# Performance work log

Hardware: AMD Instinct MI355X
Metric: run time of the kernel (lower is better)

The kernel has to match this reference:

```python
import jax, jax.numpy as jnp
import numpy as np

B, S, D, MAX_LEN = 4, 2048, 512, 2048
V = 2 * MAX_LEN + 1  # embedding table size
POS_MAX = 3000


def setup_inputs() -> dict:
    key = jax.random.key(0)
    k1, k2, k3 = jax.random.split(key, 3)
    x = jax.random.normal(k1, (B, S, D), dtype=jnp.float32)
    emb_table = jax.random.normal(k2, (V, D), dtype=jnp.float32) * 0.02
    positions = jnp.sort(jax.random.randint(k3, (B, S), 0, POS_MAX), axis=-1)
    return {"x": x, "emb_table": emb_table, "positions": positions}


def reference(x, emb_table, positions):
    # x: [B,S,D], emb_table: [2M+1, D], positions: [B,S] int
    Bc, Sc, _ = x.shape
    Vc = emb_table.shape[0]
    M = (Vc - 1) // 2
    # rel[b,i,j] = clamp(pos_i - pos_j, -M, M) + M   -> index into table
    rel = jnp.clip(positions[:, :, None] - positions[:, None, :], -M, M) + M  # [B,S,S]
    # mean_j emb[rel[b,i,j]] == (occurrence counts over V) @ table / S
    # counts[b,i,v] = #{j : rel[b,i,j] == v}; identical math, no [B,S,S,D] tensor.
    b_idx = jnp.arange(Bc)[:, None, None]
    i_idx = jnp.arange(Sc)[None, :, None]
    counts = jnp.zeros((Bc, Sc, Vc), dtype=x.dtype).at[b_idx, i_idx, rel].add(1.0)
    mean_emb = jnp.einsum('bsv,vd->bsd', counts, emb_table) / Sc  # [B,S,D]
    return x + mean_emb
```

## Files before the change

kernel.cpp:

```cpp
#include <hip/hip_runtime.h>
#include <hip/hip_bf16.h>
#include <cstdint>

#define NB 4
#define NS 2048
#define ND 512
#define NM 2048
#define NV 4097
#define NP 3000
#define RSW 3080
#define EBI_KB 129
#define HTI_BATCH_BYTES (2 * 256 * 1024)

typedef __bf16 bf16x8 __attribute__((ext_vector_type(8)));
typedef float f32x4 __attribute__((ext_vector_type(4)));

__device__ __forceinline__ unsigned short f2bf(float f) {
  union { __bf16 b; unsigned short u; } cv;
  cv.b = (__bf16)f;
  return cv.u;
}

__device__ __forceinline__ int lbound_dev(const int* a, int n, int key) {
  int lo = 0, hi = n;
  while (lo < hi) { int mid = (lo + hi) >> 1; if (a[mid] < key) lo = mid + 1; else hi = mid; }
  return lo;
}

__global__ void k_prep(const int* __restrict__ pos, const float* __restrict__ emb,
                       unsigned short* __restrict__ HTI, unsigned short* __restrict__ EBI,
                       int* __restrict__ rs) {
  __shared__ float tile[64][65];
  __shared__ unsigned int h[NP];
  int blk = blockIdx.x, tid = threadIdx.x;
  if (blk < 52) {
    int b = blk & 3, chunk = blk >> 2;
    int t = chunk * 256 + tid;
    if (t <= 3072) rs[b * RSW + t] = lbound_dev(pos + b * NS, NS, t);
    return;
  }
  if (blk < 564) {
    int idx = (blk - 52) * 256 + tid;
    int bb = idx >> 15;
    for (int i = tid; i < NP; i += 256) h[i] = 0u;
    __syncthreads();
    const int* pb = pos + bb * NS;
    for (int i = tid; i < NS; i += 256) atomicAdd(&h[pb[i]], 1u);
    __syncthreads();
    int l = idx & 63;
    int tb = (idx >> 6) & 255;
    int p = (idx >> 14) & 1;
    int base = 5104 + (l & 15) - tb * 32 - p * 16 - ((l >> 4) * 8);
    union { unsigned short us[8]; uint4 v4; } pk;
#pragma unroll
    for (int e = 0; e < 8; ++e) {
      int ii = base - e;
      float f = (ii >= 0 && ii < NP) ? (float)h[ii] : 0.0f;
      pk.us[e] = f2bf(f);
    }
    *(uint4*)(HTI + ((size_t)(bb * 2 + p) * 256 + tb) * 512 + l * 8) = pk.v4;
    return;
  }
  {
    int blk2 = blk - 564;
    int v0 = (blk2 % 65) * 64, d0 = (blk2 / 65) * 64;
    int c = tid & 63, r0 = tid >> 6;
#pragma unroll
    for (int k = 0; k < 16; ++k) {
      int r = k * 4 + r0;
      int v = v0 + r;
      float val = 0.f;
      if (v < NV && v != 0 && v != (NV - 1)) val = emb[(size_t)v * ND + d0 + c];
      tile[r][c] = val;
    }
    __syncthreads();
#pragma unroll
    for (int rep = 0; rep < 2; ++rep) {
      int tile_id = rep * 4 + (tid >> 6);
      int l = tid & 63;
      int kb_loc = tile_id >> 2, dt_loc = tile_id & 3;
      int kb = (v0 >> 5) + kb_loc, dt = (d0 >> 4) + dt_loc;
      if (kb < EBI_KB) {
        union { unsigned short us[8]; uint4 v4; } pk;
#pragma unroll
        for (int e = 0; e < 8; ++e)
          pk.us[e] = f2bf(tile[kb_loc * 32 + ((l >> 4) * 8) + e][dt_loc * 16 + (l & 15)]);
        *(uint4*)(EBI + ((size_t)dt * EBI_KB + kb) * 512 + l * 8) = pk.v4;
      }
    }
  }
}

#define LOADSET(sa0, sa1, sb0, sb1, sb2, sb3, tt)                                   \
  if ((tt) < nt) {                                                                  \
    int tof = (tt) * 1024 + vo;                                                     \
    sa0 = *(const bf16x8*)(hb + (size_t)(cA0 + tof));                               \
    sa1 = *(const bf16x8*)(hb + (size_t)(cA1 + tof));                               \
    sb0 = *(const bf16x8*)(eb + (size_t)(cB0 + tof));                               \
    sb1 = *(const bf16x8*)(eb + (size_t)(cB1 + tof));                               \
    sb2 = *(const bf16x8*)(eb + (size_t)(cB2 + tof));                               \
    sb3 = *(const bf16x8*)(eb + (size_t)(cB3 + tof));                               \
  }

#define MMSET(sa0, sa1, sb0, sb1, sb2, sb3)                                         \
  acc[0][0] = __builtin_amdgcn_mfma_f32_16x16x32_bf16(sa0, sb0, acc[0][0], 0, 0, 0);\
  acc[0][1] = __builtin_amdgcn_mfma_f32_16x16x32_bf16(sa0, sb1, acc[0][1], 0, 0, 0);\
  acc[0][2] = __builtin_amdgcn_mfma_f32_16x16x32_bf16(sa0, sb2, acc[0][2], 0, 0, 0);\
  acc[0][3] = __builtin_amdgcn_mfma_f32_16x16x32_bf16(sa0, sb3, acc[0][3], 0, 0, 0);\
  acc[1][0] = __builtin_amdgcn_mfma_f32_16x16x32_bf16(sa1, sb0, acc[1][0], 0, 0, 0);\
  acc[1][1] = __builtin_amdgcn_mfma_f32_16x16x32_bf16(sa1, sb1, acc[1][1], 0, 0, 0);\
  acc[1][2] = __builtin_amdgcn_mfma_f32_16x16x32_bf16(sa1, sb2, acc[1][2], 0, 0, 0);\
  acc[1][3] = __builtin_amdgcn_mfma_f32_16x16x32_bf16(sa1, sb3, acc[1][3], 0, 0, 0);

__global__ __launch_bounds__(256)
void k4_gemm(const unsigned short* __restrict__ HTI, const unsigned short* __restrict__ EBI,
             const int* __restrict__ rs, const float* __restrict__ x,
             const float* __restrict__ emb, float* __restrict__ out) {
  int tid = threadIdx.x, w = tid >> 6, lane = tid & 63;
  int flat = (blockIdx.x & 7) * 96 + (blockIdx.x >> 3);
  int qb = flat % 24;
  int rest = flat / 24;
  int db = rest & 7, b = rest >> 3;
  int Q0w = qb * 128 + w * 32;
  int D0w = db * 64;

  int v_lo = (Q0w > 951) ? ((Q0w - 951) & ~31) : 0;
  int v_hi = Q0w + 2080; if (v_hi > 4128) v_hi = 4128;
  int nt = (v_hi - v_lo) >> 5;

  const char* hb = (const char*)HTI + (size_t)b * HTI_BATCH_BYTES;
  const char* eb = (const char*)EBI;

  int S0 = 3056 - Q0w + v_lo;
  int S1 = S0 - 16;
  int cA0 = (((S0 >> 4) & 1) * 256 + (S0 >> 5)) * 1024;
  int cA1 = (((S1 >> 4) & 1) * 256 + (S1 >> 5)) * 1024;
  int kb0 = v_lo >> 5, dt0 = D0w >> 4;
  int cB0 = ((dt0 + 0) * EBI_KB + kb0) * 1024;
  int cB1 = ((dt0 + 1) * EBI_KB + kb0) * 1024;
  int cB2 = ((dt0 + 2) * EBI_KB + kb0) * 1024;
  int cB3 = ((dt0 + 3) * EBI_KB + kb0) * 1024;
  int vo = lane * 16;

  f32x4 acc[2][4];
#pragma unroll
  for (int a1 = 0; a1 < 2; ++a1)
#pragma unroll
    for (int a2 = 0; a2 < 4; ++a2) { f32x4 z = {0.f, 0.f, 0.f, 0.f}; acc[a1][a2] = z; }

  bf16x8 a00, a01, b00, b01, b02, b03;
  bf16x8 a10, a11, b10, b11, b12, b13;
  bf16x8 a20, a21, b20, b21, b22, b23;

  LOADSET(a00, a01, b00, b01, b02, b03, 0);
  LOADSET(a10, a11, b10, b11, b12, b13, 1);

  int t = 0;
  for (;;) {
    LOADSET(a20, a21, b20, b21, b22, b23, t + 2);
    MMSET(a00, a01, b00, b01, b02, b03);
    if (++t == nt) break;
    LOADSET(a00, a01, b00, b01, b02, b03, t + 2);
    MMSET(a10, a11, b10, b11, b12, b13);
    if (++t == nt) break;
    LOADSET(a10, a11, b10, b11, b12, b13, t + 2);
    MMSET(a20, a21, b20, b21, b22, b23);
    if (++t == nt) break;
  }

  const int* rsb = rs + b * RSW;
  const float* xb = x + (size_t)b * NS * ND;
  float* outb = out + (size_t)b * NS * ND;
  int col = lane & 15, rb4 = (lane >> 4) * 4;
#pragma unroll
  for (int nf = 0; nf < 4; ++nf) {
    int dcol = D0w + nf * 16 + col;
    float e0v = emb[dcol];
    float eMv = emb[(size_t)(NV - 1) * ND + dcol];
#pragma unroll
    for (int mf = 0; mf < 2; ++mf) {
#pragma unroll
      for (int j = 0; j < 4; ++j) {
        int q = Q0w + mf * 16 + rb4 + j;
        if (q >= NP) continue;
        int i0 = rsb[q], i1 = rsb[q + 1];
        if (i0 == i1) continue;
        int cge = (q >= NM) ? rsb[q - NM + 1] : 0;
        int cle = (q + NM < NP) ? (NS - rsb[q + NM]) : 0;
        float val = (acc[mf][nf][j] + (float)cge * eMv + (float)cle * e0v) * (1.0f / (float)NS);
        for (int i = i0; i < i1; ++i)
          outb[(size_t)i * ND + dcol] = xb[(size_t)i * ND + dcol] + val;
      }
    }
  }
}

extern "C" void kernel_launch(void* const* d_in, const int* in_sizes, int n_in,
                              void* d_out, int out_size, void* d_ws, size_t ws_size,
                              hipStream_t stream) {
  const float* x = (const float*)d_in[0];
  const float* emb = (const float*)d_in[1];
  const int* pos = (const int*)d_in[2];
  float* out = (float*)d_out;

  char* ws = (char*)d_ws;
  unsigned short* HTI = (unsigned short*)(ws);
  unsigned short* EBI = (unsigned short*)(ws + 2097152);
  int* rs = (int*)(ws + 6324224);

  hipLaunchKernelGGL(k_prep, dim3(1084), dim3(256), 0, stream, pos, emb, HTI, EBI, rs);
  hipLaunchKernelGGL(k4_gemm, dim3(768), dim3(256), 0, stream, HTI, EBI, rs, x, emb, out);
}
```

Measured before the change: 156.0 us.

## Split GEMM K-range into two halves and add separate gather-output kernel

The GEMM is split along the reduction dimension into two halves, doubling the block count to 1536, with occupancy hint 6. Each half writes a bf16 partial result per position to a workspace buffer. A new per-row kernel reads the row's position, sums the two partials, adds the boundary-count corrections and x, and writes the output with coalesced float2 stores. This replaces the scattered per-position output loop and aims to improve load balance and parallelism. The cost is an extra launch, about 12 MB of bf16 partial writes and reads, and extra rounding from storing the partials in bf16.

```diff
diff --git a/kernel.cpp b/kernel.cpp
--- a/kernel.cpp
+++ b/kernel.cpp
@@ -11,6 +11,8 @@
 #define RSW 3080
 #define EBI_KB 129
 #define HTI_BATCH_BYTES (2 * 256 * 1024)
+#define RQ 3072
+#define RHALF 6291456
 
 typedef __bf16 bf16x8 __attribute__((ext_vector_type(8)));
 typedef float f32x4 __attribute__((ext_vector_type(4)));
@@ -19,6 +21,9 @@
   union { __bf16 b; unsigned short u; } cv;
   cv.b = (__bf16)f;
   return cv.u;
+}
+__device__ __forceinline__ float bfbits2f(unsigned int u) {
+  return __uint_as_float(u << 16);
 }
 
 __device__ __forceinline__ int lbound_dev(const int* a, int n, int key) {
@@ -112,30 +117,33 @@
   acc[1][2] = __builtin_amdgcn_mfma_f32_16x16x32_bf16(sa1, sb2, acc[1][2], 0, 0, 0);\
   acc[1][3] = __builtin_amdgcn_mfma_f32_16x16x32_bf16(sa1, sb3, acc[1][3], 0, 0, 0);
 
-__global__ __launch_bounds__(256)
-void k4_gemm(const unsigned short* __restrict__ HTI, const unsigned short* __restrict__ EBI,
-             const int* __restrict__ rs, const float* __restrict__ x,
-             const float* __restrict__ emb, float* __restrict__ out) {
+__global__ __launch_bounds__(256, 6)
+void k4s_gemm(const unsigned short* __restrict__ HTI, const unsigned short* __restrict__ EBI,
+              unsigned short* __restrict__ R) {
   int tid = threadIdx.x, w = tid >> 6, lane = tid & 63;
-  int flat = (blockIdx.x & 7) * 96 + (blockIdx.x >> 3);
-  int qb = flat % 24;
-  int rest = flat / 24;
-  int db = rest & 7, b = rest >> 3;
+  int db = blockIdx.x & 7;
+  int sub = blockIdx.x >> 3;
+  int qb = sub % 24;
+  int rest = sub / 24;
+  int b = rest & 3, hh = rest >> 2;
   int Q0w = qb * 128 + w * 32;
   int D0w = db * 64;
 
   int v_lo = (Q0w > 951) ? ((Q0w - 951) & ~31) : 0;
   int v_hi = Q0w + 2080; if (v_hi > 4128) v_hi = 4128;
-  int nt = (v_hi - v_lo) >> 5;
+  int ntt = (v_hi - v_lo) >> 5;
+  int nh0 = (ntt + 1) >> 1;
+  int v_st = v_lo + (hh ? nh0 * 32 : 0);
+  int nt = hh ? (ntt - nh0) : nh0;
 
   const char* hb = (const char*)HTI + (size_t)b * HTI_BATCH_BYTES;
   const char* eb = (const char*)EBI;
 
-  int S0 = 3056 - Q0w + v_lo;
+  int S0 = 3056 - Q0w + v_st;
   int S1 = S0 - 16;
   int cA0 = (((S0 >> 4) & 1) * 256 + (S0 >> 5)) * 1024;
   int cA1 = (((S1 >> 4) & 1) * 256 + (S1 >> 5)) * 1024;
-  int kb0 = v_lo >> 5, dt0 = D0w >> 4;
+  int kb0 = v_st >> 5, dt0 = D0w >> 4;
   int cB0 = ((dt0 + 0) * EBI_KB + kb0) * 1024;
   int cB1 = ((dt0 + 1) * EBI_KB + kb0) * 1024;
   int cB2 = ((dt0 + 2) * EBI_KB + kb0) * 1024;
@@ -168,31 +176,48 @@
     if (++t == nt) break;
   }
 
-  const int* rsb = rs + b * RSW;
-  const float* xb = x + (size_t)b * NS * ND;
-  float* outb = out + (size_t)b * NS * ND;
+  unsigned short* Rh = R + (size_t)hh * RHALF + ((size_t)b * RQ) * ND;
   int col = lane & 15, rb4 = (lane >> 4) * 4;
 #pragma unroll
   for (int nf = 0; nf < 4; ++nf) {
     int dcol = D0w + nf * 16 + col;
-    float e0v = emb[dcol];
-    float eMv = emb[(size_t)(NV - 1) * ND + dcol];
 #pragma unroll
     for (int mf = 0; mf < 2; ++mf) {
 #pragma unroll
       for (int j = 0; j < 4; ++j) {
         int q = Q0w + mf * 16 + rb4 + j;
-        if (q >= NP) continue;
-        int i0 = rsb[q], i1 = rsb[q + 1];
-        if (i0 == i1) continue;
-        int cge = (q >= NM) ? rsb[q - NM + 1] : 0;
-        int cle = (q + NM < NP) ? (NS - rsb[q + NM]) : 0;
-        float val = (acc[mf][nf][j] + (float)cge * eMv + (float)cle * e0v) * (1.0f / (float)NS);
-        for (int i = i0; i < i1; ++i)
-          outb[(size_t)i * ND + dcol] = xb[(size_t)i * ND + dcol] + val;
+        Rh[(size_t)q * ND + dcol] = f2bf(acc[mf][nf][j]);
       }
     }
   }
+}
+
+__global__ __launch_bounds__(256)
+void k5_out(const int* __restrict__ pos, const int* __restrict__ rs,
+            const float* __restrict__ x, const float* __restrict__ emb,
+            const unsigned short* __restrict__ R, float* __restrict__ out) {
+  int row = blockIdx.x;
+  int b = row >> 11, i = row & 2047;
+  int q = pos[b * NS + i];
+  const int* rsb = rs + b * RSW;
+  int cge = (q >= NM) ? rsb[q - NM + 1] : 0;
+  int cle = (q + NM < NP) ? (NS - rsb[q + NM]) : 0;
+  float fg = (float)cge, fl = (float)cle;
+  int d0 = threadIdx.x * 2;
+  const unsigned short* r0 = R + ((size_t)b * RQ + q) * ND + d0;
+  const unsigned short* r1 = r0 + RHALF;
+  unsigned int u0 = *(const unsigned int*)r0;
+  unsigned int u1 = *(const unsigned int*)r1;
+  float ra = bfbits2f(u0 & 0xffffu) + bfbits2f(u1 & 0xffffu);
+  float rb = bfbits2f(u0 >> 16) + bfbits2f(u1 >> 16);
+  float e0a = emb[d0], e0b = emb[d0 + 1];
+  float eMa = emb[(size_t)(NV - 1) * ND + d0], eMb = emb[(size_t)(NV - 1) * ND + d0 + 1];
+  const float* xp = x + (size_t)row * ND + d0;
+  float2 xx = *(const float2*)xp;
+  float2 o;
+  o.x = xx.x + (ra + fg * eMa + fl * e0a) * (1.0f / (float)NS);
+  o.y = xx.y + (rb + fg * eMb + fl * e0b) * (1.0f / (float)NS);
+  *(float2*)(out + (size_t)row * ND + d0) = o;
 }
 
 extern "C" void kernel_launch(void* const* d_in, const int* in_sizes, int n_in,
@@ -204,10 +229,12 @@
   float* out = (float*)d_out;
 
   char* ws = (char*)d_ws;
-  unsigned short* HTI = (unsigned short*)(ws);
-  unsigned short* EBI = (unsigned short*)(ws + 2097152);
-  int* rs = (int*)(ws + 6324224);
+  unsigned short* R = (unsigned short*)(ws);
+  unsigned short* HTI = (unsigned short*)(ws + 25165824);
+  unsigned short* EBI = (unsigned short*)(ws + 27262976);
+  int* rs = (int*)(ws + 31490048);
 
   hipLaunchKernelGGL(k_prep, dim3(1084), dim3(256), 0, stream, pos, emb, HTI, EBI, rs);
-  hipLaunchKernelGGL(k4_gemm, dim3(768), dim3(256), 0, stream, HTI, EBI, rs, x, emb, out);
-}
+  hipLaunchKernelGGL(k4s_gemm, dim3(1536), dim3(256), 0, stream, HTI, EBI, R);
+  hipLaunchKernelGGL(k5_out, dim3(8192), dim3(256), 0, stream, pos, rs, x, emb, R, out);
+}
```

Result: slower. 452.0 us (+189.8%).
